# Kernel optimization log

Measured on AMD Instinct MI355X. Metric: run time of the kernel, lower is better.

## Reference

```python
import jax, jax.numpy as jnp
import numpy as np
from jax import lax

K_SEL = 30   # top-30 nearest voxels used for attention
K_NRM = 8    # top-8 nearest voxels used for the query normal estimate
C = 128      # output_channel
H = 1        # num_heads
DEPTH = C // H


def setup_inputs() -> dict:
    key = jax.random.key(0)
    ks = jax.random.split(key, 10)
    N, M = 8192, 16384
    x_world = jax.random.normal(ks[0], (N, 1, 3), dtype=jnp.float32)
    voxel_point = jax.random.normal(ks[1], (M, 3), dtype=jnp.float32)
    voxel_normal = jax.random.normal(ks[2], (M, 3), dtype=jnp.float32)
    v = jax.random.normal(ks[3], (M, 1), dtype=jnp.float32)
    # Linear params (torch nn.Linear: y = x @ W.T + b)
    s_fc = 1.0 / np.sqrt(6.0)
    s_c = 1.0 / np.sqrt(C)
    fc_w = jax.random.uniform(ks[4], (C, 6), jnp.float32, -s_fc, s_fc)
    fc_b = jax.random.uniform(ks[5], (C,), jnp.float32, -s_fc, s_fc)
    wq_w = jax.random.uniform(ks[6], (C, C), jnp.float32, -s_c, s_c)
    wq_b = jax.random.uniform(ks[7], (C,), jnp.float32, -s_c, s_c)
    wk_w = jax.random.uniform(ks[8], (C, C), jnp.float32, -s_c, s_c)
    wk_b = jax.random.uniform(ks[9], (C,), jnp.float32, -s_c, s_c)
    return {"x_world": x_world, "voxel_point": voxel_point, "voxel_normal": voxel_normal,
            "v": v, "fc_w": fc_w, "fc_b": fc_b, "wq_w": wq_w, "wq_b": wq_b,
            "wk_w": wk_w, "wk_b": wk_b}


def reference(x_world, voxel_point, voxel_normal, v, fc_w, fc_b, wq_w, wq_b, wk_w, wk_b):
    # x_world: [N,1,3], voxel_point/voxel_normal: [M,3], v: [M,1]
    # pairwise distances [N,M]
    dist = jnp.linalg.norm(x_world - voxel_point[None, :, :3], axis=-1)
    # top-30 nearest voxels (ascending distance == top_k of -distance)
    _, idx = lax.top_k(-dist, K_SEL)            # [N,30]
    idx8 = idx[:, :K_NRM]
    vp_sel = voxel_point[idx]                    # [N,30,3]
    vn_sel = voxel_normal[idx]                   # [N,30,3]
    v_sel = v[idx]                               # [N,30,1]
    x_normal = jnp.mean(voxel_normal[idx8], axis=1, keepdims=True)  # [N,1,3]
    normal_rel = x_normal - vn_sel               # [N,30,3]
    # mirror torch.no_grad detachment of the selected/normal tensors
    vp_sel = lax.stop_gradient(vp_sel)
    normal_rel = lax.stop_gradient(normal_rel)
    v_sel = lax.stop_gradient(v_sel)
    pos_rel = x_world - vp_sel                   # [N,30,3]
    x = jnp.concatenate([pos_rel, normal_rel], axis=-1)  # [N,30,6]
    x = x @ fc_w.T + fc_b                        # [N,30,C]
    Q = x @ wq_w.T + wq_b                        # [N,30,C] (num_heads=1 -> depth=C)
    K = x @ wk_w.T + wk_b
    scores = jnp.einsum('nkd,nld->nkl', Q, K) / np.sqrt(DEPTH).astype(np.float32)
    attn = jax.nn.softmax(scores, axis=-1)       # [N,30,30]
    out = jnp.einsum('nkl,nlo->nko', attn, v_sel)[..., 0]  # [N,30]
    return jnp.mean(out, axis=1)                 # [N]
```

## Files before the change

kernel.cpp:

```cpp
#include <hip/hip_runtime.h>
#include <math.h>
#include <float.h>

#define KSEL 30
#define KNRM 8
#define CAP  320
#define PL   320
#define G    32
#define NCELL (G*G*G)
#define GLO  (-4.8f)
#define Hc   (0.3f)
#define INVH (3.3333333333f)
#define NWAVE 2
#define NB   64

typedef unsigned long long ull;
typedef unsigned int uint;

__device__ __forceinline__ int cell_coord(float x) {
    int c = (int)floorf((x - GLO) * INVH);
    return c < 0 ? 0 : (c > G - 1 ? G - 1 : c);
}

__device__ __forceinline__ float gap1(float x, int i) {
    float lo = (i == 0)     ? -1e30f : GLO + (float)i * Hc;
    float hi = (i == G - 1) ?  1e30f : GLO + (float)(i + 1) * Hc;
    float g = 0.f;
    g = fmaxf(g, lo - x);
    g = fmaxf(g, x - hi);
    return g;
}

__device__ __forceinline__ void gbar(int* ctr, int idx) {
    __syncthreads();
    if (threadIdx.x == 0) {
        __threadfence();
        atomicAdd(&ctr[idx], 1);
        while (__hip_atomic_load(&ctr[idx], __ATOMIC_RELAXED,
                                 __HIP_MEMORY_SCOPE_AGENT) < NB) {
            __builtin_amdgcn_s_sleep(2);
        }
        __threadfence();
    }
    __syncthreads();
}

__global__ __launch_bounds__(256) void k_build(
    const float* __restrict__ vp, int* __restrict__ ctr, int* __restrict__ cc,
    int2* __restrict__ cse, float4* __restrict__ sp4, int* __restrict__ sidx,
    int* __restrict__ gpart, int M,
    const float* __restrict__ fc_w, const float* __restrict__ fc_b,
    const float* __restrict__ wq_w, const float* __restrict__ wq_b,
    const float* __restrict__ wk_w, const float* __restrict__ wk_b,
    float* __restrict__ ws)
{
    const int b   = blockIdx.x;
    const int tid = threadIdx.x;

    __shared__ int   part[256];
    __shared__ int   s_excl;
    __shared__ float Fs[768];
    __shared__ float fb[128];
    __shared__ float Gq[128][6];
    __shared__ float Gk[128][6];
    __shared__ float hq[128];

    if (b == NB) {
        for (int e = tid; e < 768; e += 256) Fs[e] = fc_w[e];
        if (tid < 128) fb[tid] = fc_b[tid];
        __syncthreads();
        const float4* wq4 = (const float4*)wq_w;
        const float4* wk4 = (const float4*)wk_w;
        for (int e = tid; e < 768; e += 256) {
            int r = e / 6, c = e % 6;
            float aq = 0.f, ak = 0.f;
            for (int k = 0; k < 32; ++k) {
                float4 a = wq4[r * 32 + k];
                float4 bb = wk4[r * 32 + k];
                aq += a.x * Fs[(4 * k + 0) * 6 + c];
                aq += a.y * Fs[(4 * k + 1) * 6 + c];
                aq += a.z * Fs[(4 * k + 2) * 6 + c];
                aq += a.w * Fs[(4 * k + 3) * 6 + c];
                ak += bb.x * Fs[(4 * k + 0) * 6 + c];
                ak += bb.y * Fs[(4 * k + 1) * 6 + c];
                ak += bb.z * Fs[(4 * k + 2) * 6 + c];
                ak += bb.w * Fs[(4 * k + 3) * 6 + c];
            }
            Gq[r][c] = aq;
            Gk[r][c] = ak;
        }
        if (tid < 128) {
            float a = wq_b[tid];
            for (int k = 0; k < 32; ++k) {
                float4 v = wq4[tid * 32 + k];
                a += v.x * fb[4 * k + 0];
                a += v.y * fb[4 * k + 1];
                a += v.z * fb[4 * k + 2];
                a += v.w * fb[4 * k + 3];
            }
            hq[tid] = a;
        }
        __syncthreads();
        const float inv_s = 0.0883883476483184f;
        if (tid < 36) {
            int a = tid / 6, bcol = tid % 6;
            float s = 0.f;
            for (int i = 0; i < 128; ++i) s += Gq[i][a] * Gk[i][bcol];
            ws[tid] = s * inv_s;
        }
        if (tid >= 64 && tid < 70) {
            int bcol = tid - 64;
            float s = 0.f;
            for (int i = 0; i < 128; ++i) s += Gk[i][bcol] * hq[i];
            ws[36 + bcol] = s * inv_s;
        }
        return;
    }

    for (int i = b * 256 + tid; i < M; i += NB * 256) {
        int cx = cell_coord(vp[i * 3 + 0]);
        int cy = cell_coord(vp[i * 3 + 1]);
        int cz = cell_coord(vp[i * 3 + 2]);
        atomicAdd(&cc[(cx * G + cy) * G + cz], 1);
    }
    gbar(ctr, 0);

    const int base = b * (NCELL / NB);
    int c0 = cc[base + 2 * tid];
    int c1 = cc[base + 2 * tid + 1];
    int s  = c0 + c1;
    part[tid] = s;
    __syncthreads();
    for (int off = 1; off < 256; off <<= 1) {
        int v = (tid >= off) ? part[tid - off] : 0;
        __syncthreads();
        part[tid] += v;
        __syncthreads();
    }
    if (tid == 255) gpart[b] = part[255];
    gbar(ctr, 1);

    if (tid < 64) {
        int v = gpart[tid];
        int inc = v;
#pragma unroll
        for (int off = 1; off < 64; off <<= 1) {
            int t = __shfl_up(inc, off, 64);
            if (tid >= off) inc += t;
        }
        if (tid == b) s_excl = inc - v;
    }
    __syncthreads();

    {
        int excl = s_excl + part[tid] - s;
        int st0 = excl, st1 = excl + c0;
        cse[base + 2 * tid]     = make_int2(st0, st0 + c0);
        cse[base + 2 * tid + 1] = make_int2(st1, st1 + c1);
        cc[base + 2 * tid]      = st0;
        cc[base + 2 * tid + 1]  = st1;
    }
    gbar(ctr, 2);

    for (int i = b * 256 + tid; i < M; i += NB * 256) {
        float x = vp[i * 3 + 0], y = vp[i * 3 + 1], z = vp[i * 3 + 2];
        int c = (cell_coord(x) * G + cell_coord(y)) * G + cell_coord(z);
        int p = atomicAdd(&cc[c], 1);
        sp4[p] = make_float4(x, y, z, 0.0f);
        sidx[p] = i;
    }
}

__global__ __launch_bounds__(64 * NWAVE) void k_main(
    const float* __restrict__ xw, const float* __restrict__ vp,
    const float* __restrict__ vn, const float* __restrict__ vv,
    const float* __restrict__ ws,
    const int2* __restrict__ cse,
    const float4* __restrict__ sp4, const int* __restrict__ sidx,
    float* __restrict__ out, int M, int N)
{
    const int tid  = threadIdx.x;
    const int lane = tid & 63;
    const int w    = tid >> 6;
    const int n    = blockIdx.x * NWAVE + w;
    const bool valid = (n < N);

    __shared__ ull            s_key[NWAVE][CAP];
    __shared__ unsigned short s_pl[NWAVE][PL];
    __shared__ float s_t[NWAVE][KSEL][6];
    __shared__ float s_vn[NWAVE][KSEL][3];
    __shared__ float s_e[NWAVE][KSEL];
    __shared__ float s_v[NWAVE][KSEL];
    __shared__ float s_o[NWAVE][KSEL];
    __shared__ int   s_sel[NWAVE][KSEL];
    __shared__ float s_xn[NWAVE][3];
    __shared__ int   s_cnt[NWAVE];
    __shared__ int   s_pn[NWAVE];
    __shared__ int   s_done[NWAVE];

    const float x0 = valid ? xw[n * 3 + 0] : 0.f;
    const float x1 = valid ? xw[n * 3 + 1] : 0.f;
    const float x2 = valid ? xw[n * 3 + 2] : 0.f;

    auto midf = [](float a, float b) -> float {
        unsigned ua = __float_as_uint(a), ub = __float_as_uint(b);
        return __uint_as_float((ua + ub) >> 1);
    };

    const float c0 = 0.063493636f * (float)M * 4.18879020f;
    float R = sqrtf(x0 * x0 + x1 * x1 + x2 * x2);
    float r = cbrtf(30.0f / (c0 * __expf(-0.5f * R * R)));
#pragma unroll
    for (int it = 0; it < 4; ++it) {
        float d  = fmaxf(R - r, 0.0f);
        float rn = cbrtf(30.0f / (c0 * __expf(-0.5f * d * d)));
        r = sqrtf(r * rn);
    }
    float T = 1.45f * r * r;

    float Tlo = 0.f, Thi = 0.f;
    bool  haveHi = false, last = false;
    bool  mydone = !valid;
    int   nc = 0;

    for (int attempt = 0; attempt < 24; ++attempt) {
        if (lane == 0) s_cnt[w] = 0;
        __syncthreads();

        if (!mydone) {
            float Tm = T * 1.000002f;
            float sq = sqrtf(T);
            int ax0 = cell_coord(x0 - sq), ax1 = cell_coord(x0 + sq);
            int ay0 = cell_coord(x1 - sq), ay1 = cell_coord(x1 + sq);
            int az0 = cell_coord(x2 - sq), az1 = cell_coord(x2 + sq);
            int nyv = ay1 - ay0 + 1, nz = az1 - az0 + 1;
            int tot = (ax1 - ax0 + 1) * nyv * nz;

            uint mz  = (nz  > 1) ? (uint)((0x100000000ULL + (ull)nz  - 1) / (ull)nz ) : 0u;
            uint myv = (nyv > 1) ? (uint)((0x100000000ULL + (ull)nyv - 1) / (ull)nyv) : 0u;

            if (lane == 0) s_pn[w] = 0;

            for (int cb = 0; cb < tot; cb += 64) {
                int ci = cb + lane;
                int rs = 0, re = 0;
                if (ci < tot) {
                    uint rest = (nz  > 1) ? __umulhi((uint)ci, mz)  : (uint)ci;
                    uint iz   = (uint)ci - rest * (uint)nz;
                    uint q2   = (nyv > 1) ? __umulhi(rest, myv) : rest;
                    uint iy   = rest - q2 * (uint)nyv;
                    int  IX = ax0 + (int)q2, IY = ay0 + (int)iy, IZ = az0 + (int)iz;
                    float gx = gap1(x0, IX), gy = gap1(x1, IY), gz = gap1(x2, IZ);
                    float mind2 = gx * gx + gy * gy + gz * gz;
                    if (mind2 <= Tm) {
                        int2 se = cse[(IX * G + IY) * G + IZ];
                        rs = se.x; re = se.y;
                    }
                }
                while (__any(rs < re)) {
                    if (rs < re) {
                        int len  = re - rs;
                        int bse  = atomicAdd(&s_pn[w], len);
                        int room = PL - bse;
                        int take = room > 0 ? (len < room ? len : room) : 0;
                        for (int i = 0; i < take; ++i)
                            s_pl[w][bse + i] = (unsigned short)(rs + i);
                        rs += take;
                    }
                    int tt = s_pn[w]; tt = tt < PL ? tt : PL;
                    for (int p = lane; p < tt; p += 64) {
                        int pidx = s_pl[w][p];
                        float4 q = sp4[pidx];
                        float dx = __fsub_rn(x0, q.x);
                        float dy = __fsub_rn(x1, q.y);
                        float dz = __fsub_rn(x2, q.z);
                        float d2 = __fadd_rn(__fadd_rn(__fmul_rn(dx, dx), __fmul_rn(dy, dy)),
                                             __fmul_rn(dz, dz));
                        if (d2 < T) {
                            int pos = atomicAdd(&s_cnt[w], 1);
                            if (pos < CAP) {
                                s_key[w][pos] = ((ull)__float_as_uint(d2) << 32) |
                                                (unsigned)sidx[pidx];
                            }
                        }
                    }
                    if (lane == 0) s_pn[w] = 0;
                }
            }
        }
        __syncthreads();

        if (!mydone) {
            nc = s_cnt[w];
            if (last || (nc >= KSEL && nc <= CAP)) {
                mydone = true;
            } else {
                if (nc < KSEL) { Tlo = T; T = haveHi ? midf(Tlo, Thi) : T * 2.5f; }
                else           { Thi = T; haveHi = true; T = midf(Tlo, Thi); }
                if (haveHi && (__float_as_uint(Thi) - __float_as_uint(Tlo) <= 1u)) {
                    T = Thi;
                    last = true;
                }
            }
        }
        if (lane == 0) s_done[w] = mydone ? 1 : 0;
        __syncthreads();
        bool alldone = true;
#pragma unroll
        for (int w2 = 0; w2 < NWAVE; ++w2) alldone = alldone && (s_done[w2] != 0);
        if (alldone) break;
    }
    if (nc > CAP) nc = CAP;

    if (lane < KSEL) s_sel[w][lane] = 0;
    __syncthreads();

    for (int i0 = lane; i0 < nc; i0 += 64) {
        ull me = s_key[w][i0];
        int rank = 0;
        for (int i = 0; i < nc; ++i) rank += (s_key[w][i] < me) ? 1 : 0;
        if (rank < KSEL) s_sel[w][rank] = (int)(me & 0xffffffffull);
    }
    __syncthreads();

    float r0 = 0.f, r1 = 0.f, r2 = 0.f;
    if (lane < KSEL) {
        int ix = s_sel[w][lane];
        r0 = __fsub_rn(x0, vp[ix * 3 + 0]);
        r1 = __fsub_rn(x1, vp[ix * 3 + 1]);
        r2 = __fsub_rn(x2, vp[ix * 3 + 2]);
        s_vn[w][lane][0] = vn[ix * 3 + 0];
        s_vn[w][lane][1] = vn[ix * 3 + 1];
        s_vn[w][lane][2] = vn[ix * 3 + 2];
        s_v[w][lane]     = vv[ix];
    }
    __syncthreads();
    if (lane == 0) {
        float a0 = 0.f, a1 = 0.f, a2 = 0.f;
        for (int k = 0; k < KNRM; ++k) {
            a0 += s_vn[w][k][0]; a1 += s_vn[w][k][1]; a2 += s_vn[w][k][2];
        }
        s_xn[w][0] = a0 * 0.125f; s_xn[w][1] = a1 * 0.125f; s_xn[w][2] = a2 * 0.125f;
    }
    __syncthreads();

    float r3 = 0.f, r4 = 0.f, r5 = 0.f;
    if (lane < KSEL) {
        r3 = __fsub_rn(s_xn[w][0], s_vn[w][lane][0]);
        r4 = __fsub_rn(s_xn[w][1], s_vn[w][lane][1]);
        r5 = __fsub_rn(s_xn[w][2], s_vn[w][lane][2]);
        float rr[6] = {r0, r1, r2, r3, r4, r5};
        float e = 0.f;
#pragma unroll
        for (int i = 0; i < 6; ++i) e += ws[36 + i] * rr[i];
        s_e[w][lane] = e;
#pragma unroll
        for (int j = 0; j < 6; ++j) {
            float t = 0.f;
#pragma unroll
            for (int i = 0; i < 6; ++i) t += ws[j * 6 + i] * rr[i];
            s_t[w][lane][j] = t;
        }
    }
    __syncthreads();

    if (lane < KSEL) {
        float sc[KSEL];
        float mx = -1e30f;
#pragma unroll
        for (int l = 0; l < KSEL; ++l) {
            float s = s_e[w][l];
            s += r0 * s_t[w][l][0];
            s += r1 * s_t[w][l][1];
            s += r2 * s_t[w][l][2];
            s += r3 * s_t[w][l][3];
            s += r4 * s_t[w][l][4];
            s += r5 * s_t[w][l][5];
            sc[l] = s;
            mx = fmaxf(mx, s);
        }
        float den = 0.f, num = 0.f;
#pragma unroll
        for (int l = 0; l < KSEL; ++l) {
            float wgt = __expf(sc[l] - mx);
            den += wgt;
            num += wgt * s_v[w][l];
        }
        s_o[w][lane] = num / den;
    }
    __syncthreads();

    if (lane == 0 && valid) {
        float a = 0.f;
        for (int k = 0; k < KSEL; ++k) a += s_o[w][k];
        out[n] = a * (1.0f / 30.0f);
    }
}

extern "C" void kernel_launch(void* const* d_in, const int* in_sizes, int n_in,
                              void* d_out, int out_size, void* d_ws, size_t ws_size,
                              hipStream_t stream)
{
    const float* xw   = (const float*)d_in[0];
    const float* vp   = (const float*)d_in[1];
    const float* vn   = (const float*)d_in[2];
    const float* vv   = (const float*)d_in[3];
    const float* fc_w = (const float*)d_in[4];
    const float* fc_b = (const float*)d_in[5];
    const float* wq_w = (const float*)d_in[6];
    const float* wq_b = (const float*)d_in[7];
    const float* wk_w = (const float*)d_in[8];
    const float* wk_b = (const float*)d_in[9];

    int N = in_sizes[0] / 3;
    int M = in_sizes[1] / 3;

    float*  ws_f  = (float*)d_ws;
    int*    ctr   = (int*)(ws_f + 64);
    int*    cc    = ctr + 16;
    int2*   cse   = (int2*)(cc + NCELL);
    float4* sp4   = (float4*)(cse + NCELL);
    int*    sidx  = (int*)(sp4 + M);
    int*    gpart = sidx + M;

    hipMemsetAsync(ctr, 0, (16 + NCELL) * sizeof(int), stream);

    k_build<<<NB + 1, 256, 0, stream>>>(vp, ctr, cc, cse, sp4, sidx, gpart, M,
                                        fc_w, fc_b, wq_w, wq_b, wk_w, wk_b, ws_f);
    k_main<<<(N + NWAVE - 1) / NWAVE, 64 * NWAVE, 0, stream>>>(
        xw, vp, vn, vv, ws_f, cse, sp4, sidx, (float*)d_out, M, N);
}
```

Before: 88.76 us.

## Split kNN selection into a persistent work-stealing kernel and a separate attention kernel

Splits the fused kernel into k_select and k_attn. k_select is a persistent kernel whose waves pull query points from a global atomic counter, so a fast wave no longer waits for its slower partner to finish the radius search. It writes the 30 selected indices to a buffer that k_attn reads, and k_attn runs with 4 waves per block. The original voxel index is packed into the w component of sp4, which removes the separate sidx gather. Indices are stored as 16-bit values, which only holds while M stays at or below 65536, and the change adds a kernel launch plus a global round trip for the selections.

```diff
diff --git a/kernel.cpp b/kernel.cpp
--- a/kernel.cpp
+++ b/kernel.cpp
@@ -12,6 +12,7 @@
 #define Hc   (0.3f)
 #define INVH (3.3333333333f)
 #define NWAVE 2
+#define AWAVE 4
 #define NB   64
 
 typedef unsigned long long ull;
@@ -47,7 +48,7 @@
 
 __global__ __launch_bounds__(256) void k_build(
     const float* __restrict__ vp, int* __restrict__ ctr, int* __restrict__ cc,
-    int2* __restrict__ cse, float4* __restrict__ sp4, int* __restrict__ sidx,
+    int2* __restrict__ cse, float4* __restrict__ sp4,
     int* __restrict__ gpart, int M,
     const float* __restrict__ fc_w, const float* __restrict__ fc_b,
     const float* __restrict__ wq_w, const float* __restrict__ wq_b,
@@ -166,41 +167,25 @@
         float x = vp[i * 3 + 0], y = vp[i * 3 + 1], z = vp[i * 3 + 2];
         int c = (cell_coord(x) * G + cell_coord(y)) * G + cell_coord(z);
         int p = atomicAdd(&cc[c], 1);
-        sp4[p] = make_float4(x, y, z, 0.0f);
-        sidx[p] = i;
-    }
-}
-
-__global__ __launch_bounds__(64 * NWAVE) void k_main(
-    const float* __restrict__ xw, const float* __restrict__ vp,
-    const float* __restrict__ vn, const float* __restrict__ vv,
-    const float* __restrict__ ws,
-    const int2* __restrict__ cse,
-    const float4* __restrict__ sp4, const int* __restrict__ sidx,
-    float* __restrict__ out, int M, int N)
+        sp4[p] = make_float4(x, y, z, __int_as_float(i));
+    }
+}
+
+__global__ __launch_bounds__(64 * NWAVE) void k_select(
+    const float* __restrict__ xw,
+    const int2* __restrict__ cse, const float4* __restrict__ sp4,
+    int* __restrict__ gctr, unsigned short* __restrict__ selout,
+    int M, int N)
 {
     const int tid  = threadIdx.x;
     const int lane = tid & 63;
     const int w    = tid >> 6;
-    const int n    = blockIdx.x * NWAVE + w;
-    const bool valid = (n < N);
 
     __shared__ ull            s_key[NWAVE][CAP];
     __shared__ unsigned short s_pl[NWAVE][PL];
-    __shared__ float s_t[NWAVE][KSEL][6];
-    __shared__ float s_vn[NWAVE][KSEL][3];
-    __shared__ float s_e[NWAVE][KSEL];
-    __shared__ float s_v[NWAVE][KSEL];
-    __shared__ float s_o[NWAVE][KSEL];
-    __shared__ int   s_sel[NWAVE][KSEL];
-    __shared__ float s_xn[NWAVE][3];
     __shared__ int   s_cnt[NWAVE];
     __shared__ int   s_pn[NWAVE];
     __shared__ int   s_done[NWAVE];
-
-    const float x0 = valid ? xw[n * 3 + 0] : 0.f;
-    const float x1 = valid ? xw[n * 3 + 1] : 0.f;
-    const float x2 = valid ? xw[n * 3 + 2] : 0.f;
 
     auto midf = [](float a, float b) -> float {
         unsigned ua = __float_as_uint(a), ub = __float_as_uint(b);
@@ -208,26 +193,42 @@
     };
 
     const float c0 = 0.063493636f * (float)M * 4.18879020f;
-    float R = sqrtf(x0 * x0 + x1 * x1 + x2 * x2);
-    float r = cbrtf(30.0f / (c0 * __expf(-0.5f * R * R)));
-#pragma unroll
-    for (int it = 0; it < 4; ++it) {
-        float d  = fmaxf(R - r, 0.0f);
-        float rn = cbrtf(30.0f / (c0 * __expf(-0.5f * d * d)));
-        r = sqrtf(r * rn);
-    }
-    float T = 1.45f * r * r;
-
-    float Tlo = 0.f, Thi = 0.f;
+
+    bool  idle = false, haspt = false;
+    int   n = -1, attempts = 0;
+    float x0 = 0.f, x1 = 0.f, x2 = 0.f;
+    float T = 1.f, Tlo = 0.f, Thi = 0.f;
     bool  haveHi = false, last = false;
-    bool  mydone = !valid;
-    int   nc = 0;
-
-    for (int attempt = 0; attempt < 24; ++attempt) {
+
+    for (int iter = 0; iter < 16384; ++iter) {
+        if (!idle && !haspt) {
+            int nn = 0;
+            if (lane == 0) nn = atomicAdd(gctr, 1);
+            nn = __shfl(nn, 0, 64);
+            if (nn < N) {
+                n = nn; haspt = true;
+                x0 = xw[n * 3 + 0];
+                x1 = xw[n * 3 + 1];
+                x2 = xw[n * 3 + 2];
+                float R = sqrtf(x0 * x0 + x1 * x1 + x2 * x2);
+                float r = cbrtf(30.0f / (c0 * __expf(-0.5f * R * R)));
+#pragma unroll
+                for (int it = 0; it < 4; ++it) {
+                    float d  = fmaxf(R - r, 0.0f);
+                    float rn = cbrtf(30.0f / (c0 * __expf(-0.5f * d * d)));
+                    r = sqrtf(r * rn);
+                }
+                T = 1.45f * r * r;
+                Tlo = 0.f; Thi = 0.f; haveHi = false; last = false; attempts = 0;
+            } else {
+                idle = true;
+            }
+        }
+
         if (lane == 0) s_cnt[w] = 0;
         __syncthreads();
 
-        if (!mydone) {
+        if (haspt) {
             float Tm = T * 1.000002f;
             float sq = sqrtf(T);
             int ax0 = cell_coord(x0 - sq), ax1 = cell_coord(x0 + sq);
@@ -280,7 +281,7 @@
                             int pos = atomicAdd(&s_cnt[w], 1);
                             if (pos < CAP) {
                                 s_key[w][pos] = ((ull)__float_as_uint(d2) << 32) |
-                                                (unsigned)sidx[pidx];
+                                                (unsigned)__float_as_int(q.w);
                             }
                         }
                     }
@@ -290,10 +291,20 @@
         }
         __syncthreads();
 
-        if (!mydone) {
-            nc = s_cnt[w];
-            if (last || (nc >= KSEL && nc <= CAP)) {
-                mydone = true;
+        if (haspt) {
+            int nc = s_cnt[w];
+            ++attempts;
+            bool accept = last || (nc >= KSEL && nc <= CAP) || (attempts >= 24);
+            if (accept) {
+                if (nc > CAP) nc = CAP;
+                for (int i0 = lane; i0 < nc; i0 += 64) {
+                    ull me = s_key[w][i0];
+                    int rank = 0;
+                    for (int i = 0; i < nc; ++i) rank += (s_key[w][i] < me) ? 1 : 0;
+                    if (rank < KSEL)
+                        selout[n * 32 + rank] = (unsigned short)(me & 0xffffull);
+                }
+                haspt = false;
             } else {
                 if (nc < KSEL) { Tlo = T; T = haveHi ? midf(Tlo, Thi) : T * 2.5f; }
                 else           { Thi = T; haveHi = true; T = midf(Tlo, Thi); }
@@ -303,29 +314,43 @@
                 }
             }
         }
-        if (lane == 0) s_done[w] = mydone ? 1 : 0;
+
+        if (lane == 0) s_done[w] = idle ? 1 : 0;
         __syncthreads();
         bool alldone = true;
 #pragma unroll
         for (int w2 = 0; w2 < NWAVE; ++w2) alldone = alldone && (s_done[w2] != 0);
         if (alldone) break;
     }
-    if (nc > CAP) nc = CAP;
-
-    if (lane < KSEL) s_sel[w][lane] = 0;
-    __syncthreads();
-
-    for (int i0 = lane; i0 < nc; i0 += 64) {
-        ull me = s_key[w][i0];
-        int rank = 0;
-        for (int i = 0; i < nc; ++i) rank += (s_key[w][i] < me) ? 1 : 0;
-        if (rank < KSEL) s_sel[w][rank] = (int)(me & 0xffffffffull);
-    }
-    __syncthreads();
+}
+
+__global__ __launch_bounds__(64 * AWAVE) void k_attn(
+    const float* __restrict__ xw, const float* __restrict__ vp,
+    const float* __restrict__ vn, const float* __restrict__ vv,
+    const float* __restrict__ ws, const unsigned short* __restrict__ selout,
+    float* __restrict__ out, int M, int N)
+{
+    const int tid  = threadIdx.x;
+    const int lane = tid & 63;
+    const int w    = tid >> 6;
+    const int n    = blockIdx.x * AWAVE + w;
+    const bool valid = (n < N);
+
+    __shared__ float s_t[AWAVE][KSEL][6];
+    __shared__ float s_vn[AWAVE][KSEL][3];
+    __shared__ float s_e[AWAVE][KSEL];
+    __shared__ float s_v[AWAVE][KSEL];
+    __shared__ float s_o[AWAVE][KSEL];
+    __shared__ float s_xn[AWAVE][3];
+
+    const float x0 = valid ? xw[n * 3 + 0] : 0.f;
+    const float x1 = valid ? xw[n * 3 + 1] : 0.f;
+    const float x2 = valid ? xw[n * 3 + 2] : 0.f;
 
     float r0 = 0.f, r1 = 0.f, r2 = 0.f;
-    if (lane < KSEL) {
-        int ix = s_sel[w][lane];
+    if (lane < KSEL && valid) {
+        int ix = (int)selout[n * 32 + lane];
+        if (ix >= M) ix = 0;
         r0 = __fsub_rn(x0, vp[ix * 3 + 0]);
         r1 = __fsub_rn(x1, vp[ix * 3 + 1]);
         r2 = __fsub_rn(x2, vp[ix * 3 + 2]);
@@ -415,18 +440,23 @@
     int N = in_sizes[0] / 3;
     int M = in_sizes[1] / 3;
 
-    float*  ws_f  = (float*)d_ws;
-    int*    ctr   = (int*)(ws_f + 64);
-    int*    cc    = ctr + 16;
-    int2*   cse   = (int2*)(cc + NCELL);
-    float4* sp4   = (float4*)(cse + NCELL);
-    int*    sidx  = (int*)(sp4 + M);
-    int*    gpart = sidx + M;
+    float*          ws_f   = (float*)d_ws;
+    int*            ctr    = (int*)(ws_f + 64);
+    int*            cc     = ctr + 16;
+    int2*           cse    = (int2*)(cc + NCELL);
+    float4*         sp4    = (float4*)(cse + NCELL);
+    unsigned short* selout = (unsigned short*)(sp4 + M);
+    int*            gpart  = (int*)(selout + (size_t)N * 32);
 
     hipMemsetAsync(ctr, 0, (16 + NCELL) * sizeof(int), stream);
 
-    k_build<<<NB + 1, 256, 0, stream>>>(vp, ctr, cc, cse, sp4, sidx, gpart, M,
+    k_build<<<NB + 1, 256, 0, stream>>>(vp, ctr, cc, cse, sp4, gpart, M,
                                         fc_w, fc_b, wq_w, wq_b, wk_w, wk_b, ws_f);
-    k_main<<<(N + NWAVE - 1) / NWAVE, 64 * NWAVE, 0, stream>>>(
-        xw, vp, vn, vv, ws_f, cse, sp4, sidx, (float*)d_out, M, N);
-}
+
+    int selBlocks = 2048;
+    k_select<<<selBlocks, 64 * NWAVE, 0, stream>>>(
+        xw, cse, sp4, &ctr[8], selout, M, N);
+
+    k_attn<<<(N + AWAVE - 1) / AWAVE, 64 * AWAVE, 0, stream>>>(
+        xw, vp, vn, vv, ws_f, selout, (float*)d_out, M, N);
+}
```

Result: slower. 216.9 us (+144.3%).
